# Optimization experiments

Hardware: AMD Instinct MI355X
Metric: run time of the kernel (lower is better)

Reference implementation:

```python
import jax, jax.numpy as jnp
import numpy as np

D_MODEL, D_STATE, EXPAND = 1024, 16, 2
D_INNER = EXPAND * D_MODEL
BATCH, SEQ = 4, 4096


def setup_inputs() -> dict:
    key = jax.random.key(0)
    ks = jax.random.split(key, 9)
    s = 0.02
    return {
        "x": jax.random.normal(ks[0], (BATCH, SEQ, D_MODEL), jnp.float32),
        # torch Linear weight [out,in] stored transposed here as [in,out]
        "W_in": jax.random.normal(ks[1], (D_MODEL, 2 * D_INNER), jnp.float32) * s,
        "conv_w": jax.random.normal(ks[2], (D_INNER, 1, 3), jnp.float32) * s,  # depthwise, groups=D_INNER
        "conv_b": jax.random.normal(ks[3], (D_INNER,), jnp.float32) * s,
        "W_B": jax.random.normal(ks[4], (D_INNER, D_STATE), jnp.float32) * s,
        "W_C": jax.random.normal(ks[5], (D_INNER, D_STATE), jnp.float32) * s,
        "A": jax.random.normal(ks[6], (D_STATE,), jnp.float32),
        "D": jnp.ones((D_INNER,), jnp.float32),
        "W_out": jax.random.normal(ks[7], (D_INNER, D_MODEL), jnp.float32) * s,
    }


def reference(x, W_in, conv_w, conv_b, W_B, W_C, A, D, W_out):
    d_inner = conv_w.shape[0]
    # input projection and split into main / residual gate paths
    xr = jnp.einsum("bld,de->ble", x, W_in)  # [B, L, 2*d_inner]
    x_main, res = xr[..., :d_inner], xr[..., d_inner:]
    # depthwise conv1d along seq (kernel 3, pad 1)
    xc = jax.lax.conv_general_dilated(
        x_main.transpose(0, 2, 1), conv_w, (1,), [(1, 1)],
        dimension_numbers=("NCH", "OIH", "NCH"), feature_group_count=d_inner)
    xc = (xc + conv_b[None, :, None]).transpose(0, 2, 1)  # [B, L, d_inner]
    xc = jax.nn.silu(xc)
    # selective-scan inputs
    Bt = jnp.einsum("bli,is->bls", xc, W_B)  # [B, L, d_state]
    Ct = jnp.einsum("bli,is->bls", xc, W_C)
    decay = jnp.exp(-jax.nn.softplus(A))  # exp(A_diag), [d_state]

    def step(state, bc):
        b_t, c_t = bc
        state = state * decay + b_t  # i=0: zeros*decay + B[0] == B[0]
        return state, jnp.sum(state * c_t, axis=-1)  # scalar per batch

    _, ys = jax.lax.scan(step, jnp.zeros_like(Bt[:, 0]),
                         (Bt.transpose(1, 0, 2), Ct.transpose(1, 0, 2)))
    ys = ys.T  # [B, L]
    y = ys[..., None] + xc * D  # broadcast scan output across d_inner
    y = y * jax.nn.silu(res)
    return jnp.einsum("bli,id->bld", y, W_out)
```

## Files before the change

kernel.cpp:

```cpp
#include <hip/hip_runtime.h>


typedef _Float16 half8 __attribute__((ext_vector_type(8)));
typedef float floatx4 __attribute__((ext_vector_type(4)));

#define D_MODEL 1024
#define D_INNER 2048
#define SEQ     4096
#define NBATCH  4
#define NROWS   (NBATCH * SEQ)
#define CHUNK   16
#define NCHUNK  (SEQ / CHUNK)
#define NTASK   (NBATCH * NCHUNK)

__device__ __forceinline__ void async16(_Float16* lds, const _Float16* g) {
    __builtin_amdgcn_global_load_lds((const __attribute__((address_space(1))) void*)g,
                                     (__attribute__((address_space(3))) void*)lds, 16, 0, 0);
}

__device__ __forceinline__ float siluf(float x) {
    return x / (1.f + __expf(-x));
}

__device__ __forceinline__ float decay_of(const float* A, int s) {
    return __expf(-log1pf(__expf(A[s])));
}


__global__ __launch_bounds__(256) void convert_f32_f16(const float* __restrict__ src,
                                                       _Float16* __restrict__ dst) {
    size_t idx = ((size_t)blockIdx.x * 256 + threadIdx.x) * 8;
    float4 a = *(const float4*)(src + idx);
    float4 b = *(const float4*)(src + idx + 4);
    half8 o = {(_Float16)a.x, (_Float16)a.y, (_Float16)a.z, (_Float16)a.w,
               (_Float16)b.x, (_Float16)b.y, (_Float16)b.z, (_Float16)b.w};
    *(half8*)(dst + idx) = o;
}

__global__ __launch_bounds__(256) void transpose_to_f16(const float* __restrict__ src,
                                                        _Float16* __restrict__ dst,
                                                        int K, int N) {
    __shared__ float tile[32][33];
    int n0 = blockIdx.x * 32, k0 = blockIdx.y * 32;
    int x = threadIdx.x, y = threadIdx.y;
#pragma unroll
    for (int r = 0; r < 32; r += 8)
        tile[y + r][x] = src[(size_t)(k0 + y + r) * N + (n0 + x)];
    __syncthreads();
#pragma unroll
    for (int r = 0; r < 32; r += 8)
        dst[(size_t)(n0 + y + r) * K + (k0 + x)] = (_Float16)tile[x][y + r];
}

__global__ __launch_bounds__(256) void convert_wbct(const float* __restrict__ WB,
                                                    const float* __restrict__ WC,
                                                    _Float16* __restrict__ WBCT) {
    int idx = blockIdx.x * 256 + threadIdx.x;
    int n = idx >> 11, k = idx & 2047;
    float v = (n < 16) ? WB[k * 16 + n] : WC[k * 16 + (n - 16)];
    WBCT[idx] = (_Float16)v;
}

template <typename OutT>
__global__ __launch_bounds__(256) void gemm_tn(const _Float16* __restrict__ A,
                                               const _Float16* __restrict__ BT,
                                               OutT* __restrict__ C,
                                               int M, int N, int K) {
    __shared__ __align__(16) _Float16 As[128 * 64];
    __shared__ __align__(16) _Float16 Bs[128 * 64];
    const int tid = threadIdx.x;
    const int wid = tid >> 6, lane = tid & 63;
    const int row0 = blockIdx.y * 128, col0 = blockIdx.x * 128;
    const int wm = (wid & 1) * 64, wn = (wid >> 1) * 64;

    floatx4 acc[4][4] = {};

    const int sr = lane >> 3;
    const int sc = ((lane & 7) ^ sr) * 8;
    const size_t aBase = (size_t)(row0 + wid * 32 + sr) * K + sc;
    const size_t bBase = (size_t)(col0 + wid * 32 + sr) * K + sc;
    _Float16* ldsA = As + wid * 2048;
    _Float16* ldsB = Bs + wid * 2048;

    const int fr = lane & 15, q = lane >> 4;
    const int frq = fr & 7;

    for (int k0 = 0; k0 < K; k0 += 64) {
        __syncthreads();
#pragma unroll
        for (int t = 0; t < 4; t++) {
            async16(ldsA + t * 512, A + aBase + (size_t)(t * 8) * K + k0);
            async16(ldsB + t * 512, BT + bBase + (size_t)(t * 8) * K + k0);
        }
        __syncthreads();
#pragma unroll
        for (int kk = 0; kk < 2; kk++) {
            const int sw = (((kk << 2) + q) ^ frq) * 8;
            half8 af[4], bf[4];
#pragma unroll
            for (int i = 0; i < 4; i++) {
                af[i] = *(const half8*)(As + (wm + i * 16 + fr) * 64 + sw);
                bf[i] = *(const half8*)(Bs + (wn + i * 16 + fr) * 64 + sw);
            }
#pragma unroll
            for (int i = 0; i < 4; i++)
#pragma unroll
                for (int j = 0; j < 4; j++)
                    acc[i][j] = __builtin_amdgcn_mfma_f32_16x16x32_f16(af[i], bf[j], acc[i][j], 0, 0, 0);
        }
    }

    const int er = (lane >> 4) * 4, ec = lane & 15;
#pragma unroll
    for (int i = 0; i < 4; i++)
#pragma unroll
        for (int j = 0; j < 4; j++)
#pragma unroll
            for (int r = 0; r < 4; r++) {
                int row = row0 + wm + i * 16 + er + r;
                int col = col0 + wn + j * 16 + ec;
                C[(size_t)row * N + col] = (OutT)acc[i][j][r];
            }
}

__global__ __launch_bounds__(256) void conv_bc_fin(const _Float16* __restrict__ xr,
                                                   const float* __restrict__ cw,
                                                   const float* __restrict__ cb,
                                                   const _Float16* __restrict__ WBCT,
                                                   const float* __restrict__ A,
                                                   _Float16* __restrict__ xc,
                                                   float* __restrict__ BtCt,
                                                   float* __restrict__ fin) {
    __shared__ __align__(16) _Float16 As[4 * 32 * 128];
    const int tid = threadIdx.x, wid = tid >> 6, lane = tid & 63;
    const int row0 = blockIdx.x * 32;
    const int l0 = row0 & (SEQ - 1);
    const int cg = lane & 15;
    const int rg = lane >> 4;
    const int fr = lane & 15, q = lane >> 4;
    _Float16* As_w = As + wid * 4096;
    const int r0 = rg * 8;

    floatx4 acc[2][2] = {};

    for (int t = 0; t < 4; t++) {
        const int kbase = wid * 512 + t * 128;
        const int gcol = kbase + cg * 8;
        float w0[8], w1[8], w2[8], bb[8];
#pragma unroll
        for (int j = 0; j < 8; j++) {
            w0[j] = cw[(gcol + j) * 3];
            w1[j] = cw[(gcol + j) * 3 + 1];
            w2[j] = cw[(gcol + j) * 3 + 2];
            bb[j] = cb[gcol + j];
        }
        half8 prev = {}, cur, nxt;
        if (!(l0 == 0 && rg == 0))
            prev = *(const half8*)(xr + (size_t)(row0 + r0 - 1) * 4096 + gcol);
        cur = *(const half8*)(xr + (size_t)(row0 + r0) * 4096 + gcol);
#pragma unroll
        for (int r = 0; r < 8; r++) {
            if (r == 7 && rg == 3 && l0 + 32 == SEQ) {
                half8 z = {};
                nxt = z;
            } else {
                nxt = *(const half8*)(xr + (size_t)(row0 + r0 + r + 1) * 4096 + gcol);
            }
            half8 o;
#pragma unroll
            for (int j = 0; j < 8; j++) {
                float a = (float)prev[j] * w0[j] + (float)cur[j] * w1[j] +
                          (float)nxt[j] * w2[j] + bb[j];
                o[j] = (_Float16)siluf(a);
            }
            const int lrow = r0 + r;
            *(half8*)(xc + (size_t)(row0 + lrow) * D_INNER + gcol) = o;
            *(half8*)(As_w + lrow * 128 + ((cg ^ (lrow & 7)) * 8)) = o;
            prev = cur;
            cur = nxt;
        }
#pragma unroll
        for (int ks = 0; ks < 4; ks++) {
            half8 af[2], bf[2];
#pragma unroll
            for (int rt = 0; rt < 2; rt++)
                af[rt] = *(const half8*)(As_w + (rt * 16 + fr) * 128 +
                                         (((ks * 4 + q) ^ (fr & 7)) * 8));
#pragma unroll
            for (int ot = 0; ot < 2; ot++)
                bf[ot] = *(const half8*)(WBCT + (size_t)(ot * 16 + fr) * D_INNER +
                                         kbase + ks * 32 + q * 8);
#pragma unroll
            for (int rt = 0; rt < 2; rt++)
#pragma unroll
                for (int ot = 0; ot < 2; ot++)
                    acc[rt][ot] = __builtin_amdgcn_mfma_f32_16x16x32_f16(af[rt], bf[ot], acc[rt][ot], 0, 0, 0);
        }
    }

    __syncthreads();
    float* red = (float*)As;
    float* btl = (float*)As + 4096;
    const int er = (lane >> 4) * 4, ec = lane & 15;
#pragma unroll
    for (int rt = 0; rt < 2; rt++)
#pragma unroll
        for (int ot = 0; ot < 2; ot++)
#pragma unroll
            for (int rr = 0; rr < 4; rr++)
                red[wid * 1024 + (rt * 16 + er + rr) * 32 + ot * 16 + ec] = acc[rt][ot][rr];
    __syncthreads();
#pragma unroll
    for (int i = 0; i < 4; i++) {
        int idx = i * 256 + tid;
        float v = red[idx] + red[1024 + idx] + red[2048 + idx] + red[3072 + idx];
        btl[idx] = v;
        BtCt[(size_t)row0 * 32 + idx] = v;
    }
    __syncthreads();
    if (tid < 32) {
        const int ch = tid >> 4, s = tid & 15;
        const float decay = decay_of(A, s);
        float st = 0.f;
#pragma unroll
        for (int r = 0; r < CHUNK; r++)
            st = st * decay + btl[(ch * 16 + r) * 32 + s];
        fin[((row0 >> 4) + ch) * 16 + s] = st;
    }
}

__global__ __launch_bounds__(64) void scan_p2(const float* __restrict__ fin,
                                              const float* __restrict__ A,
                                              float* __restrict__ carry) {
    int t = threadIdx.x;
    int b = t >> 4, s = t & 15;
    float decay = decay_of(A, s);
    float d16 = decay;
#pragma unroll
    for (int k = 0; k < 4; k++) d16 *= d16;
    float cy = 0.f;
#pragma unroll 8
    for (int c = 0; c < NCHUNK; c++) {
        int idx = ((b * NCHUNK) + c) * 16 + s;
        carry[idx] = cy;
        cy = cy * d16 + fin[idx];
    }
}

__global__ __launch_bounds__(256) void scan_p3_fuse(const float* __restrict__ BtCt,
                                                    const float* __restrict__ A,
                                                    const float* __restrict__ carry,
                                                    const float* __restrict__ D,
                                                    const _Float16* __restrict__ xr,
                                                    _Float16* __restrict__ xc) {
    __shared__ float ysl[CHUNK];
    const int task = blockIdx.x;
    const int b = task >> 8, c = task & (NCHUNK - 1);
    const int row0 = b * SEQ + c * CHUNK;
    const int tid = threadIdx.x;

    if (tid < 16) {
        const int s = tid;
        const float decay = decay_of(A, s);
        size_t r = (size_t)row0 * 32;
        float bt[CHUNK], ct[CHUNK];
#pragma unroll
        for (int j = 0; j < CHUNK; j++) {
            bt[j] = BtCt[r + (size_t)j * 32 + s];
            ct[j] = BtCt[r + (size_t)j * 32 + 16 + s];
        }
        float st = carry[task * 16 + s];
        float yv[CHUNK];
#pragma unroll
        for (int j = 0; j < CHUNK; j++) {
            st = st * decay + bt[j];
            yv[j] = st * ct[j];
        }
#pragma unroll
        for (int j = 0; j < CHUNK; j++) {
            float y = yv[j];
            y += __shfl_xor(y, 1, 16);
            y += __shfl_xor(y, 2, 16);
            y += __shfl_xor(y, 4, 16);
            y += __shfl_xor(y, 8, 16);
            if (s == 0) ysl[j] = y;
        }
    }
    __syncthreads();

#pragma unroll
    for (int it = 0; it < 16; it++) {
        int chunk = it * 256 + tid;
        int rl = chunk >> 8;
        int colb = (chunk & 255) * 8;
        size_t row = (size_t)(row0 + rl);
        float yv = ysl[rl];
        half8 x8 = *(const half8*)(xc + row * D_INNER + colb);
        half8 r8 = *(const half8*)(xr + row * 4096 + 2048 + colb);
        float4 d0 = *(const float4*)(D + colb);
        float4 d1 = *(const float4*)(D + colb + 4);
        half8 o;
        float dd[8] = {d0.x, d0.y, d0.z, d0.w, d1.x, d1.y, d1.z, d1.w};
#pragma unroll
        for (int j = 0; j < 8; j++) {
            float y = yv + (float)x8[j] * dd[j];
            o[j] = (_Float16)(y * siluf((float)r8[j]));
        }
        *(half8*)(xc + row * D_INNER + colb) = o;
    }
}

extern "C" void kernel_launch(void* const* d_in, const int* in_sizes, int n_in,
                              void* d_out, int out_size, void* d_ws, size_t ws_size,
                              hipStream_t stream) {
    const float* x      = (const float*)d_in[0];
    const float* W_in   = (const float*)d_in[1];
    const float* conv_w = (const float*)d_in[2];
    const float* conv_b = (const float*)d_in[3];
    const float* W_B    = (const float*)d_in[4];
    const float* W_C    = (const float*)d_in[5];
    const float* A      = (const float*)d_in[6];
    const float* D      = (const float*)d_in[7];
    const float* W_out  = (const float*)d_in[8];
    float* out = (float*)d_out;

    char* ws = (char*)d_ws;
    size_t off = 0;
    auto alloc = [&](size_t bytes) { size_t o = off; off += (bytes + 255) & ~(size_t)255; return o; };
    _Float16* xh    = (_Float16*)(ws + alloc((size_t)NROWS * D_MODEL * 2));
    _Float16* WinT  = (_Float16*)(ws + alloc((size_t)4096 * 1024 * 2));
    _Float16* WoutT = (_Float16*)(ws + alloc((size_t)1024 * 2048 * 2));
    _Float16* WBCT  = (_Float16*)(ws + alloc((size_t)32 * 2048 * 2));
    _Float16* xr    = (_Float16*)(ws + alloc((size_t)NROWS * 4096 * 2));
    _Float16* xc    = (_Float16*)(ws + alloc((size_t)NROWS * D_INNER * 2));
    float*    BtCt  = (float*)(ws + alloc((size_t)NROWS * 32 * 4));
    float*    fin   = (float*)(ws + alloc((size_t)NTASK * 16 * 4));
    float*    carry = (float*)(ws + alloc((size_t)NTASK * 16 * 4));

    convert_f32_f16<<<(NROWS * D_MODEL) / (256 * 8), 256, 0, stream>>>(x, xh);
    transpose_to_f16<<<dim3(4096 / 32, 1024 / 32), dim3(32, 8), 0, stream>>>(W_in, WinT, 1024, 4096);
    transpose_to_f16<<<dim3(1024 / 32, 2048 / 32), dim3(32, 8), 0, stream>>>(W_out, WoutT, 2048, 1024);
    convert_wbct<<<(32 * 2048) / 256, 256, 0, stream>>>(W_B, W_C, WBCT);
    gemm_tn<_Float16><<<dim3(4096 / 128, 64), 256, 0, stream>>>(xh, WinT, xr, NROWS / 2, 4096, 1024);
    gemm_tn<_Float16><<<dim3(4096 / 128, 64), 256, 0, stream>>>(xh + (size_t)8192 * 1024, WinT,
                                                                xr + (size_t)8192 * 4096, NROWS / 2, 4096, 1024);
    conv_bc_fin<<<NROWS / 32, 256, 0, stream>>>(xr, conv_w, conv_b, WBCT, A, xc, BtCt, fin);
    scan_p2<<<1, 64, 0, stream>>>(fin, A, carry);
    scan_p3_fuse<<<NTASK, 256, 0, stream>>>(BtCt, A, carry, D, xr, xc);
    gemm_tn<float><<<dim3(1024 / 128, NROWS / 128), 256, 0, stream>>>(xc, WoutT, out, NROWS, 1024, 2048);
}
```

Measured before the change: 475.2 us.

## Replace 128x128 GEMM with pipelined 256x256 tile kernel using double-buffered LDS

```diff
diff --git a/kernel.cpp b/kernel.cpp
--- a/kernel.cpp
+++ b/kernel.cpp
@@ -61,65 +61,124 @@
     WBCT[idx] = (_Float16)v;
 }
 
+
+__device__ __forceinline__ void stage_half(const _Float16* __restrict__ src, int K,
+                                           int rowBase, int k0, _Float16* ldsHalf) {
+    const int tid = threadIdx.x;
+    const int sr = tid >> 3, wid = tid >> 6;
+    const int lc = ((tid & 7) ^ (sr & 7)) << 3;
+#pragma unroll
+    for (int r = 0; r < 2; r++) {
+        const _Float16* g = src + (size_t)(rowBase + r * 64 + sr) * K + (k0 + lc);
+        async16(ldsHalf + r * 4096 + wid * 512, g);
+    }
+}
+
+#define GP_LOAD(MQ, NQ, LOADA)                                                          \
+    if (LOADA) {                                                                        \
+        _Pragma("unroll") for (int m = 0; m < 4; m++) {                                 \
+            const int lr = (MQ) * 128 + wm * 64 + m * 16 + fr;                          \
+            _Pragma("unroll") for (int s = 0; s < 2; s++)                               \
+                af[m][s] = *(const half8*)(Ab + lr * 64 + ((((s << 2) + q) ^ frq) << 3)); \
+        }                                                                               \
+    }                                                                                   \
+    {                                                                                   \
+        _Pragma("unroll") for (int n = 0; n < 2; n++) {                                 \
+            const int br = (NQ) * 128 + wn * 32 + n * 16 + fr;                          \
+            _Pragma("unroll") for (int s = 0; s < 2; s++)                               \
+                bf[n][s] = *(const half8*)(Bb + br * 64 + ((((s << 2) + q) ^ frq) << 3)); \
+        }                                                                               \
+    }
+
+#define GP_MMA(MQ, NQ)                                                                  \
+    __builtin_amdgcn_s_barrier();                                                       \
+    asm volatile("s_waitcnt lgkmcnt(0)" ::: "memory");                                  \
+    __builtin_amdgcn_s_setprio(1);                                                      \
+    _Pragma("unroll") for (int m = 0; m < 4; m++)                                       \
+        _Pragma("unroll") for (int n = 0; n < 2; n++)                                   \
+            _Pragma("unroll") for (int s = 0; s < 2; s++)                               \
+                acc[(MQ) * 4 + m][(NQ) * 2 + n] = __builtin_amdgcn_mfma_f32_16x16x32_f16( \
+                    af[m][s], bf[n][s], acc[(MQ) * 4 + m][(NQ) * 2 + n], 0, 0, 0);      \
+    __builtin_amdgcn_s_setprio(0);                                                      \
+    __builtin_amdgcn_s_barrier();
+
 template <typename OutT>
-__global__ __launch_bounds__(256) void gemm_tn(const _Float16* __restrict__ A,
-                                               const _Float16* __restrict__ BT,
-                                               OutT* __restrict__ C,
-                                               int M, int N, int K) {
-    __shared__ __align__(16) _Float16 As[128 * 64];
-    __shared__ __align__(16) _Float16 Bs[128 * 64];
+__global__ __launch_bounds__(512, 2) void gemm256(const _Float16* __restrict__ A,
+                                                  const _Float16* __restrict__ BT,
+                                                  OutT* __restrict__ C,
+                                                  int M, int N, int K) {
+    __shared__ __align__(16) _Float16 smem[4 * 16384];
+    _Float16* const AsBase = smem;
+    _Float16* const BsBase = smem + 32768;
+
     const int tid = threadIdx.x;
     const int wid = tid >> 6, lane = tid & 63;
-    const int row0 = blockIdx.y * 128, col0 = blockIdx.x * 128;
-    const int wm = (wid & 1) * 64, wn = (wid >> 1) * 64;
-
-    floatx4 acc[4][4] = {};
-
-    const int sr = lane >> 3;
-    const int sc = ((lane & 7) ^ sr) * 8;
-    const size_t aBase = (size_t)(row0 + wid * 32 + sr) * K + sc;
-    const size_t bBase = (size_t)(col0 + wid * 32 + sr) * K + sc;
-    _Float16* ldsA = As + wid * 2048;
-    _Float16* ldsB = Bs + wid * 2048;
-
-    const int fr = lane & 15, q = lane >> 4;
-    const int frq = fr & 7;
-
-    for (int k0 = 0; k0 < K; k0 += 64) {
-        __syncthreads();
-#pragma unroll
-        for (int t = 0; t < 4; t++) {
-            async16(ldsA + t * 512, A + aBase + (size_t)(t * 8) * K + k0);
-            async16(ldsB + t * 512, BT + bBase + (size_t)(t * 8) * K + k0);
-        }
-        __syncthreads();
-#pragma unroll
-        for (int kk = 0; kk < 2; kk++) {
-            const int sw = (((kk << 2) + q) ^ frq) * 8;
-            half8 af[4], bf[4];
-#pragma unroll
-            for (int i = 0; i < 4; i++) {
-                af[i] = *(const half8*)(As + (wm + i * 16 + fr) * 64 + sw);
-                bf[i] = *(const half8*)(Bs + (wn + i * 16 + fr) * 64 + sw);
-            }
-#pragma unroll
-            for (int i = 0; i < 4; i++)
-#pragma unroll
-                for (int j = 0; j < 4; j++)
-                    acc[i][j] = __builtin_amdgcn_mfma_f32_16x16x32_f16(af[i], bf[j], acc[i][j], 0, 0, 0);
-        }
+    const int wm = wid >> 2, wn = wid & 3;
+    const int fr = lane & 15, q = lane >> 4, frq = fr & 7;
+
+    int lin = blockIdx.y * gridDim.x + blockIdx.x;
+    const int nwg = gridDim.x * gridDim.y;
+    lin = (lin & 7) * (nwg >> 3) + (lin >> 3);
+    const int bx = lin % gridDim.x, by = lin / gridDim.x;
+    const int row0 = by * 256, col0 = bx * 256;
+    const int NT = K >> 6;
+
+    floatx4 acc[8][4] = {};
+    half8 af[4][2], bf[2][2];
+
+    stage_half(A,  K, row0,       0, AsBase);
+    stage_half(BT, K, col0,       0, BsBase);
+    stage_half(A,  K, row0 + 128, 0, AsBase + 8192);
+    stage_half(BT, K, col0 + 128, 0, BsBase + 8192);
+    if (NT > 1) {
+        stage_half(A,  K, row0, 64, AsBase + 16384);
+        stage_half(BT, K, col0, 64, BsBase + 16384);
+        asm volatile("s_waitcnt vmcnt(4)" ::: "memory");
+    } else {
+        asm volatile("s_waitcnt vmcnt(0)" ::: "memory");
+    }
+    __builtin_amdgcn_s_barrier();
+
+    for (int t = 0; t < NT; ++t) {
+        _Float16* Ab  = AsBase + ((t & 1) << 14);
+        _Float16* Bb  = BsBase + ((t & 1) << 14);
+        _Float16* Abn = AsBase + (((t + 1) & 1) << 14);
+        _Float16* Bbn = BsBase + (((t + 1) & 1) << 14);
+        const int k1 = (t + 1) << 6, k2 = (t + 2) << 6;
+        const bool s1 = (t + 1) < NT, s2 = (t + 2) < NT;
+
+        GP_LOAD(0, 0, 1);
+        if (s1) stage_half(A, K, row0 + 128, k1, Abn + 8192);
+        GP_MMA(0, 0);
+
+        GP_LOAD(0, 1, 0);
+        if (s1) stage_half(BT, K, col0 + 128, k1, Bbn + 8192);
+        GP_MMA(0, 1);
+
+        GP_LOAD(1, 0, 1);
+        if (s2) stage_half(A, K, row0, k2, Ab);
+        GP_MMA(1, 0);
+
+        GP_LOAD(1, 1, 0);
+        if (s2) stage_half(BT, K, col0, k2, Bb);
+        if (s2) {
+            asm volatile("s_waitcnt vmcnt(4)" ::: "memory");
+        } else if (t + 2 == NT) {
+            asm volatile("s_waitcnt vmcnt(0)" ::: "memory");
+        }
+        GP_MMA(1, 1);
     }
 
     const int er = (lane >> 4) * 4, ec = lane & 15;
 #pragma unroll
-    for (int i = 0; i < 4; i++)
-#pragma unroll
-        for (int j = 0; j < 4; j++)
+    for (int fi = 0; fi < 8; fi++)
+#pragma unroll
+        for (int fj = 0; fj < 4; fj++)
 #pragma unroll
             for (int r = 0; r < 4; r++) {
-                int row = row0 + wm + i * 16 + er + r;
-                int col = col0 + wn + j * 16 + ec;
-                C[(size_t)row * N + col] = (OutT)acc[i][j][r];
+                int row = row0 + (fi >> 2) * 128 + wm * 64 + (fi & 3) * 16 + er + r;
+                int col = col0 + (fj >> 1) * 128 + wn * 32 + (fj & 1) * 16 + ec;
+                C[(size_t)row * N + col] = (OutT)acc[fi][fj][r];
             }
 }
 
@@ -341,11 +400,9 @@
     transpose_to_f16<<<dim3(4096 / 32, 1024 / 32), dim3(32, 8), 0, stream>>>(W_in, WinT, 1024, 4096);
     transpose_to_f16<<<dim3(1024 / 32, 2048 / 32), dim3(32, 8), 0, stream>>>(W_out, WoutT, 2048, 1024);
     convert_wbct<<<(32 * 2048) / 256, 256, 0, stream>>>(W_B, W_C, WBCT);
-    gemm_tn<_Float16><<<dim3(4096 / 128, 64), 256, 0, stream>>>(xh, WinT, xr, NROWS / 2, 4096, 1024);
-    gemm_tn<_Float16><<<dim3(4096 / 128, 64), 256, 0, stream>>>(xh + (size_t)8192 * 1024, WinT,
-                                                                xr + (size_t)8192 * 4096, NROWS / 2, 4096, 1024);
+    gemm256<_Float16><<<dim3(4096 / 256, NROWS / 256), 512, 0, stream>>>(xh, WinT, xr, NROWS, 4096, 1024);
     conv_bc_fin<<<NROWS / 32, 256, 0, stream>>>(xr, conv_w, conv_b, WBCT, A, xc, BtCt, fin);
     scan_p2<<<1, 64, 0, stream>>>(fin, A, carry);
     scan_p3_fuse<<<NTASK, 256, 0, stream>>>(BtCt, A, carry, D, xr, xc);
-    gemm_tn<float><<<dim3(1024 / 128, NROWS / 128), 256, 0, stream>>>(xc, WoutT, out, NROWS, 1024, 2048);
-}
+    gemm256<float><<<dim3(1024 / 256, NROWS / 256), 512, 0, stream>>>(xc, WoutT, out, NROWS, 1024, 2048);
+}
```

Measured after the change: 450.0 us. -5.3%, faster.
